# Optimization experiments

Hardware: AMD Instinct MI355X
Metric: run time of the kernel (lower is better)

## Reference

```python
import jax, jax.numpy as jnp
import numpy as np
from jax import lax

MB, NS, Z_DIM, R_DIM, HID, NUM_STEPS = 128, 64, 64, 128, 512, 100
B = MB * NS
T_TOTAL = 1.0
ETA = 1.0
DT = T_TOTAL / NUM_STEPS
LOG2PI = float(np.log(2.0 * np.pi))


def setup_inputs() -> dict:
    key = jax.random.key(0)
    ks = jax.random.split(key, 8)
    in_dim = Z_DIM + R_DIM + 1
    return {
        "r": jax.random.normal(ks[0], (MB, NS, R_DIM), jnp.float32),
        "noises": jax.random.normal(ks[1], (B, NUM_STEPS, Z_DIM), jnp.float32),
        "x0": jax.random.normal(ks[2], (B, Z_DIM), jnp.float32) * ETA,  # prior sample, std=eta
        "W1": jax.random.normal(ks[3], (in_dim, HID), jnp.float32) / np.sqrt(in_dim),
        "b1": jnp.zeros((HID,), jnp.float32),
        "W2": jax.random.normal(ks[4], (HID, Z_DIM), jnp.float32) / np.sqrt(HID),
        "b2": jnp.zeros((Z_DIM,), jnp.float32),
        "beta_max": jnp.float32(10.0),
        "beta_min": jnp.float32(0.01),
        "target_mu": jax.random.normal(ks[5], (Z_DIM,), jnp.float32),
    }


def reference(r, noises, x0, W1, b1, W2, b2, beta_max, beta_min, target_mu):
    # cosine-squared schedule (analytic integrals), per update_schedules()
    C_start = jax.nn.softplus(beta_max)
    C_end = jax.nn.softplus(beta_min)
    a = C_start - C_end
    b = jnp.pi / (2.0 * T_TOTAL)
    c = C_end

    def F(t):  # forward integrated scheduler \int_0^t
        return a * jnp.sin(2.0 * b * t) / (4.0 * b) + a * t / 2.0 + c * t

    steps = jnp.arange(NUM_STEPS + 1, dtype=jnp.float32)
    alpha = 1.0 - jnp.exp(-2.0 * (F((steps + 1.0) * DT) - F(steps * DT)))  # [S+1]
    kappa = (ETA * (1.0 - jnp.sqrt(1.0 - alpha))) ** 2 / alpha              # [S+1]

    r_flat = r.reshape(B, R_DIM)

    def control(t, x):  # score network: MLP on concat(x, r, t)
        t_feat = jnp.full((B, 1), t, dtype=x.dtype)
        h = jnp.tanh(jnp.concatenate([x, r_flat, t_feat], axis=-1) @ W1 + b1)
        return h @ W2 + b2

    def step(carry, xs):
        x, lw = carry
        t, al, ka, noise = xs
        score = control(t, x)
        means = x + (1.0 - jnp.sqrt(1.0 - al)) * (2.0 * ETA ** 2 * score - x)
        std = ETA * jnp.sqrt(al)
        x_new = means + std * noise
        lw_det = -2.0 * ka * jnp.sum(score ** 2, axis=-1)
        lw_sto = -2.0 * jnp.sqrt(ka) * jnp.sum(score * noise, axis=-1)
        return (x_new, lw + lw_det + lw_sto), x_new

    xs = (
        jnp.arange(NUM_STEPS, dtype=jnp.float32) * DT,
        alpha[:NUM_STEPS],
        kappa[:NUM_STEPS],
        jnp.swapaxes(noises, 0, 1),  # [S, B, D]
    )
    (x, lw), x_hist = lax.scan(step, (x0, jnp.zeros((B,), x0.dtype)), xs)

    x_t = jnp.swapaxes(jnp.concatenate([x0[None], x_hist], axis=0), 0, 1)  # [B, S+1, D]

    # terminal weight: log target - log prior (both diagonal Normals)
    target_lp = jnp.sum(-0.5 * (x - target_mu) ** 2 - 0.5 * LOG2PI, axis=-1)
    prior_lp = jnp.sum(-0.5 * (x / ETA) ** 2 - 0.5 * LOG2PI - jnp.log(jnp.float32(ETA)), axis=-1)
    log_weights = lw + target_lp - prior_lp

    # nabla_g = prior_score(x) - target_score(x)
    nabla_g = (-x / ETA ** 2) - (-(x - target_mu))
    return x_t, log_weights, nabla_g
```

## Files before the change

kernel.cpp:

```cpp
#include <hip/hip_runtime.h>

#define ZD 64
#define RD 128
#define HIDDEN 512
#define NSTEP 100
#define OUT_PITCH 6464
#define DT_F 0.01f
#define ROWS 32

static const size_t LW_OFF = 52953088ull;
static const size_t NG_OFF = 52961280ull;

typedef __attribute__((ext_vector_type(2))) float  f32x2;
typedef __attribute__((ext_vector_type(4))) float  f32x4;
typedef __attribute__((ext_vector_type(8))) __bf16 bf16x8;
typedef __attribute__((ext_vector_type(2))) short  s16x2;
typedef __attribute__((ext_vector_type(4))) short  s16x4;
typedef __attribute__((ext_vector_type(8))) short  s16x8;

__device__ __forceinline__ short f2bs(float f) {
    return __builtin_bit_cast(short, (__bf16)f);
}
__device__ __forceinline__ float tanh_fast(float x) {
    float e = __builtin_amdgcn_exp2f(x * 2.88539008177793f);
    float r = __builtin_amdgcn_rcpf(e + 1.0f);
    return fmaf(-2.0f, r, 1.0f);
}

__global__ __launch_bounds__(1024, 1)
void sim_kernel(
    const float* __restrict__ r, const float* __restrict__ noises,
    const float* __restrict__ x0, const float* __restrict__ W1,
    const float* __restrict__ b1, const float* __restrict__ W2,
    const float* __restrict__ b2, const float* __restrict__ bmax,
    const float* __restrict__ bmin, const float* __restrict__ mu,
    float* __restrict__ out)
{
    __shared__ float Ps[2][ROWS][68];
    __shared__ unsigned short Xb[ROWS * 64];
    __shared__ unsigned short Hs[ROWS * HIDDEN];
    __shared__ float w1ts[HIDDEN];
    __shared__ float mus[ZD];
    __shared__ float b2s[ZD];
    __shared__ float tT[NSTEP], tG[NSTEP], tSd[NSTEP], tCd[NSTEP], tCs[NSTEP];

    const int tid  = threadIdx.x;
    const int lane = tid & 63;
    const int wave = tid >> 6;
    const int g4   = lane >> 4;
    const int l16  = lane & 15;
    const int row0 = blockIdx.x * ROWS;

    if (tid < NSTEP) {
        float spmax = log1pf(expf(bmax[0]));
        float spmin = log1pf(expf(bmin[0]));
        float a_ = spmax - spmin;
        float c_ = spmin;
        const float PI_ = 3.14159265358979323846f;
        float k = (float)tid;
        float t0 = k * DT_F, t1 = (k + 1.0f) * DT_F;
        float inv2pi = 1.0f / (2.0f * PI_);
        float F0 = a_ * sinf(PI_ * t0) * inv2pi + (0.5f * a_ + c_) * t0;
        float F1 = a_ * sinf(PI_ * t1) * inv2pi + (0.5f * a_ + c_) * t1;
        float al = 1.0f - expf(-2.0f * (F1 - F0));
        float gg = 1.0f - sqrtf(1.0f - al);
        float kap = (gg * gg) / al;
        tT[tid] = t0; tG[tid] = gg; tSd[tid] = sqrtf(al);
        tCd[tid] = -2.0f * kap; tCs[tid] = -2.0f * sqrtf(kap);
    }
    if (tid < HIDDEN) w1ts[tid] = W1[(size_t)192 * HIDDEN + tid];
    if (tid < ZD) { mus[tid] = mu[tid]; b2s[tid] = b2[tid]; }

    const int urow = tid >> 5;
    const int c2   = (tid & 31) * 2;
    const size_t ubase = (size_t)(row0 + urow);
    float xr0, xr1;
    {
        f32x2 v = *(const f32x2*)(x0 + ubase * ZD + c2);
        xr0 = v[0]; xr1 = v[1];
        *(f32x2*)(out + ubase * OUT_PITCH + c2) = v;
        s16x2 xv; xv[0] = f2bs(xr0); xv[1] = f2bs(xr1);
        *(s16x2*)(Xb + ((urow * 64 + c2) ^ ((urow & 7) << 3))) = xv;
    }

    f32x4 pref[2][2];
    {
        #pragma unroll
        for (int mt = 0; mt < 2; ++mt) {
            bf16x8 rf[4];
            const float* rp = r + (size_t)(row0 + mt * 16 + l16) * RD;
            #pragma unroll
            for (int kc = 0; kc < 4; ++kc) {
                f32x4 lo = *(const f32x4*)(rp + kc * 32 + g4 * 8);
                f32x4 hi = *(const f32x4*)(rp + kc * 32 + g4 * 8 + 4);
                bf16x8 v;
                v[0]=(__bf16)lo[0]; v[1]=(__bf16)lo[1]; v[2]=(__bf16)lo[2]; v[3]=(__bf16)lo[3];
                v[4]=(__bf16)hi[0]; v[5]=(__bf16)hi[1]; v[6]=(__bf16)hi[2]; v[7]=(__bf16)hi[3];
                rf[kc] = v;
            }
            #pragma unroll
            for (int j2 = 0; j2 < 2; ++j2) {
                int n  = (wave * 2 + j2) * 16 + l16;
                int n0 = (wave * 2 + j2) * 16 + g4 * 4;
                f32x4 acc = *(const f32x4*)(b1 + n0);
                #pragma unroll
                for (int kc = 0; kc < 4; ++kc) {
                    bf16x8 w;
                    #pragma unroll
                    for (int j = 0; j < 8; ++j)
                        w[j] = (__bf16)W1[(size_t)(64 + kc * 32 + g4 * 8 + j) * HIDDEN + n];
                    acc = __builtin_amdgcn_mfma_f32_16x16x32_bf16(w, rf[kc], acc, 0, 0, 0);
                }
                pref[j2][mt] = acc;
            }
        }
    }

    bf16x8 w1f[2][2];
    #pragma unroll
    for (int j2 = 0; j2 < 2; ++j2) {
        int n = (wave * 2 + j2) * 16 + l16;
        #pragma unroll
        for (int kc = 0; kc < 2; ++kc) {
            bf16x8 v;
            #pragma unroll
            for (int j = 0; j < 8; ++j) {
                int kk = kc * 32 + g4 * 8 + j;
                v[j] = (__bf16)W1[(size_t)kk * HIDDEN + n];
            }
            w1f[j2][kc] = v;
        }
    }
    const int zt = wave & 3, kh = (wave >> 2) & 1, mt2 = wave >> 3;
    bf16x8 w2f[8];
    {
        int n = zt * 16 + l16;
        #pragma unroll
        for (int i = 0; i < 8; ++i) {
            int kc = kh * 8 + i;
            bf16x8 v;
            #pragma unroll
            for (int j = 0; j < 8; ++j) {
                int kk = kc * 32 + g4 * 8 + j;
                v[j] = (__bf16)W2[(size_t)kk * ZD + n];
            }
            w2f[i] = v;
        }
    }

    float lw_acc = 0.0f;

    __syncthreads();

    for (int s = 0; s < NSTEP; ++s) {
        float t = tT[s], gg = tG[s], sdv = tSd[s], cd = tCd[s], cs = tCs[s];
        f32x2 nz = *(const f32x2*)(noises + (ubase * NSTEP + s) * ZD + c2);

        {
            s16x8 xb[2][2];
            #pragma unroll
            for (int mt = 0; mt < 2; ++mt) {
                int m = mt * 16 + l16;
                int swz = (m & 7) << 3;
                xb[mt][0] = *(const s16x8*)(Xb + ((m * 64 + g4 * 8) ^ swz));
                xb[mt][1] = *(const s16x8*)(Xb + ((m * 64 + 32 + g4 * 8) ^ swz));
            }
            #pragma unroll
            for (int j2 = 0; j2 < 2; ++j2) {
                int n0 = (wave * 2 + j2) * 16 + g4 * 4;
                f32x4 wt = *(const f32x4*)(w1ts + n0);
                #pragma unroll
                for (int mt = 0; mt < 2; ++mt) {
                    f32x4 acc = pref[j2][mt];
                    acc[0] = fmaf(t, wt[0], acc[0]);
                    acc[1] = fmaf(t, wt[1], acc[1]);
                    acc[2] = fmaf(t, wt[2], acc[2]);
                    acc[3] = fmaf(t, wt[3], acc[3]);
                    acc = __builtin_amdgcn_mfma_f32_16x16x32_bf16(
                        w1f[j2][0], __builtin_bit_cast(bf16x8, xb[mt][0]), acc, 0, 0, 0);
                    acc = __builtin_amdgcn_mfma_f32_16x16x32_bf16(
                        w1f[j2][1], __builtin_bit_cast(bf16x8, xb[mt][1]), acc, 0, 0, 0);
                    s16x4 hv;
                    hv[0] = f2bs(tanh_fast(acc[0]));
                    hv[1] = f2bs(tanh_fast(acc[1]));
                    hv[2] = f2bs(tanh_fast(acc[2]));
                    hv[3] = f2bs(tanh_fast(acc[3]));
                    int m = mt * 16 + l16;
                    *(s16x4*)(Hs + ((m * HIDDEN + n0) ^ ((m & 7) << 3))) = hv;
                }
            }
        }
        __syncthreads();

        {
            int m = mt2 * 16 + l16;
            int swz = (m & 7) << 3;
            f32x4 accA = { 0.f, 0.f, 0.f, 0.f };
            f32x4 accB = { 0.f, 0.f, 0.f, 0.f };
            int base = m * HIDDEN + kh * 256 + g4 * 8;
            #pragma unroll
            for (int i = 0; i < 8; i += 2) {
                s16x8 h0 = *(const s16x8*)(Hs + ((base + i * 32) ^ swz));
                accA = __builtin_amdgcn_mfma_f32_16x16x32_bf16(
                    w2f[i], __builtin_bit_cast(bf16x8, h0), accA, 0, 0, 0);
                s16x8 h1 = *(const s16x8*)(Hs + ((base + (i + 1) * 32) ^ swz));
                accB = __builtin_amdgcn_mfma_f32_16x16x32_bf16(
                    w2f[i + 1], __builtin_bit_cast(bf16x8, h1), accB, 0, 0, 0);
            }
            accA[0] += accB[0]; accA[1] += accB[1];
            accA[2] += accB[2]; accA[3] += accB[3];
            *(f32x4*)(&Ps[kh][m][zt * 16 + g4 * 4]) = accA;
        }
        __syncthreads();

        {
            f32x2 p0 = *(const f32x2*)(&Ps[0][urow][c2]);
            f32x2 p1 = *(const f32x2*)(&Ps[1][urow][c2]);
            f32x2 bb = *(const f32x2*)(&b2s[c2]);
            float s0 = p0[0] + p1[0] + bb[0];
            float s1 = p0[1] + p1[1] + bb[1];
            float xn0 = xr0 + gg * (2.0f * s0 - xr0) + sdv * nz[0];
            float xn1 = xr1 + gg * (2.0f * s1 - xr1) + sdv * nz[1];
            xr0 = xn0; xr1 = xn1;
            f32x2 xv = { xn0, xn1 };
            *(f32x2*)(out + ubase * OUT_PITCH + (size_t)(s + 1) * ZD + c2) = xv;
            s16x2 xb2; xb2[0] = f2bs(xn0); xb2[1] = f2bs(xn1);
            *(s16x2*)(Xb + ((urow * 64 + c2) ^ ((urow & 7) << 3))) = xb2;
            float v = cd * (s0 * s0 + s1 * s1) + cs * (s0 * nz[0] + s1 * nz[1]);
            v += __shfl_xor(v, 1, 64);
            v += __shfl_xor(v, 2, 64);
            v += __shfl_xor(v, 4, 64);
            v += __shfl_xor(v, 8, 64);
            v += __shfl_xor(v, 16, 64);
            lw_acc += v;
        }
        __syncthreads();
    }

    {
        float m0 = mus[c2], m1 = mus[c2 + 1];
        float d0 = xr0 - m0, d1 = xr1 - m1;
        f32x2 ng = { d0 - xr0, d1 - xr1 };
        *(f32x2*)(out + NG_OFF + ubase * ZD + c2) = ng;
        float part = 0.5f * (xr0 * xr0 + xr1 * xr1) - 0.5f * (d0 * d0 + d1 * d1);
        part += __shfl_xor(part, 1, 64);
        part += __shfl_xor(part, 2, 64);
        part += __shfl_xor(part, 4, 64);
        part += __shfl_xor(part, 8, 64);
        part += __shfl_xor(part, 16, 64);
        if ((tid & 31) == 0) out[LW_OFF + ubase] = lw_acc + part;
    }
}

extern "C" void kernel_launch(void* const* d_in, const int* in_sizes, int n_in,
                              void* d_out, int out_size, void* d_ws, size_t ws_size,
                              hipStream_t stream) {
    const float* r      = (const float*)d_in[0];
    const float* noises = (const float*)d_in[1];
    const float* x0     = (const float*)d_in[2];
    const float* W1     = (const float*)d_in[3];
    const float* b1     = (const float*)d_in[4];
    const float* W2     = (const float*)d_in[5];
    const float* b2     = (const float*)d_in[6];
    const float* bmax   = (const float*)d_in[7];
    const float* bmin   = (const float*)d_in[8];
    const float* mu     = (const float*)d_in[9];
    float* out = (float*)d_out;

    sim_kernel<<<256, 1024, 0, stream>>>(r, noises, x0, W1, b1, W2, b2,
                                         bmax, bmin, mu, out);
}
```

Baseline: 260.8 us.

## Split second GEMM over four K-quarters and defer log-weight reduction

Reworks how the 16 waves split the H@W2 GEMM. Each wave now covers two output column tiles over a quarter of K, so one LDS read of H feeds two MFMAs, and partial results go to four partial buffers instead of two. The per-step cross-lane shuffle reduction of the log-weight term is dropped: each lane keeps a private sum and the reduction happens once at the end. b2 and mu are read straight into registers, which removes their LDS staging. The epilogue now reads four partial buffers per step instead of two, and summation order changes slightly.

```diff
diff --git a/kernel.cpp b/kernel.cpp
--- a/kernel.cpp
+++ b/kernel.cpp
@@ -36,12 +36,10 @@
     const float* __restrict__ bmin, const float* __restrict__ mu,
     float* __restrict__ out)
 {
-    __shared__ float Ps[2][ROWS][68];
+    __shared__ float Ps[4][ROWS][72];
     __shared__ unsigned short Xb[ROWS * 64];
     __shared__ unsigned short Hs[ROWS * HIDDEN];
     __shared__ float w1ts[HIDDEN];
-    __shared__ float mus[ZD];
-    __shared__ float b2s[ZD];
     __shared__ float tT[NSTEP], tG[NSTEP], tSd[NSTEP], tCd[NSTEP], tCs[NSTEP];
 
     const int tid  = threadIdx.x;
@@ -69,7 +67,6 @@
         tCd[tid] = -2.0f * kap; tCs[tid] = -2.0f * sqrtf(kap);
     }
     if (tid < HIDDEN) w1ts[tid] = W1[(size_t)192 * HIDDEN + tid];
-    if (tid < ZD) { mus[tid] = mu[tid]; b2s[tid] = b2[tid]; }
 
     const int urow = tid >> 5;
     const int c2   = (tid & 31) * 2;
@@ -82,13 +79,14 @@
         s16x2 xv; xv[0] = f2bs(xr0); xv[1] = f2bs(xr1);
         *(s16x2*)(Xb + ((urow * 64 + c2) ^ ((urow & 7) << 3))) = xv;
     }
+    const float bb0 = b2[c2], bb1 = b2[c2 + 1];
 
     f32x4 pref[2][2];
     {
         #pragma unroll
-        for (int mt = 0; mt < 2; ++mt) {
+        for (int mtt = 0; mtt < 2; ++mtt) {
             bf16x8 rf[4];
-            const float* rp = r + (size_t)(row0 + mt * 16 + l16) * RD;
+            const float* rp = r + (size_t)(row0 + mtt * 16 + l16) * RD;
             #pragma unroll
             for (int kc = 0; kc < 4; ++kc) {
                 f32x4 lo = *(const f32x4*)(rp + kc * 32 + g4 * 8);
@@ -111,7 +109,7 @@
                         w[j] = (__bf16)W1[(size_t)(64 + kc * 32 + g4 * 8 + j) * HIDDEN + n];
                     acc = __builtin_amdgcn_mfma_f32_16x16x32_bf16(w, rf[kc], acc, 0, 0, 0);
                 }
-                pref[j2][mt] = acc;
+                pref[j2][mtt] = acc;
             }
         }
     }
@@ -131,61 +129,59 @@
             w1f[j2][kc] = v;
         }
     }
-    const int zt = wave & 3, kh = (wave >> 2) & 1, mt2 = wave >> 3;
-    bf16x8 w2f[8];
-    {
-        int n = zt * 16 + l16;
+    const int zh = wave & 1, kq = (wave >> 1) & 3, mtw = wave >> 3;
+    bf16x8 w2f[2][4];
+    #pragma unroll
+    for (int zt2 = 0; zt2 < 2; ++zt2) {
+        int n = (zh * 2 + zt2) * 16 + l16;
         #pragma unroll
-        for (int i = 0; i < 8; ++i) {
-            int kc = kh * 8 + i;
+        for (int i = 0; i < 4; ++i) {
             bf16x8 v;
             #pragma unroll
-            for (int j = 0; j < 8; ++j) {
-                int kk = kc * 32 + g4 * 8 + j;
-                v[j] = (__bf16)W2[(size_t)kk * ZD + n];
-            }
-            w2f[i] = v;
-        }
-    }
-
-    float lw_acc = 0.0f;
+            for (int j = 0; j < 8; ++j)
+                v[j] = (__bf16)W2[(size_t)(kq * 128 + i * 32 + g4 * 8 + j) * ZD + n];
+            w2f[zt2][i] = v;
+        }
+    }
+
+    float lwacc = 0.0f;
 
     __syncthreads();
 
     for (int s = 0; s < NSTEP; ++s) {
-        float t = tT[s], gg = tG[s], sdv = tSd[s], cd = tCd[s], cs = tCs[s];
+        float t = tT[s];
         f32x2 nz = *(const f32x2*)(noises + (ubase * NSTEP + s) * ZD + c2);
 
         {
             s16x8 xb[2][2];
             #pragma unroll
-            for (int mt = 0; mt < 2; ++mt) {
-                int m = mt * 16 + l16;
+            for (int mtt = 0; mtt < 2; ++mtt) {
+                int m = mtt * 16 + l16;
                 int swz = (m & 7) << 3;
-                xb[mt][0] = *(const s16x8*)(Xb + ((m * 64 + g4 * 8) ^ swz));
-                xb[mt][1] = *(const s16x8*)(Xb + ((m * 64 + 32 + g4 * 8) ^ swz));
+                xb[mtt][0] = *(const s16x8*)(Xb + ((m * 64 + g4 * 8) ^ swz));
+                xb[mtt][1] = *(const s16x8*)(Xb + ((m * 64 + 32 + g4 * 8) ^ swz));
             }
             #pragma unroll
             for (int j2 = 0; j2 < 2; ++j2) {
                 int n0 = (wave * 2 + j2) * 16 + g4 * 4;
                 f32x4 wt = *(const f32x4*)(w1ts + n0);
                 #pragma unroll
-                for (int mt = 0; mt < 2; ++mt) {
-                    f32x4 acc = pref[j2][mt];
+                for (int mtt = 0; mtt < 2; ++mtt) {
+                    f32x4 acc = pref[j2][mtt];
                     acc[0] = fmaf(t, wt[0], acc[0]);
                     acc[1] = fmaf(t, wt[1], acc[1]);
                     acc[2] = fmaf(t, wt[2], acc[2]);
                     acc[3] = fmaf(t, wt[3], acc[3]);
                     acc = __builtin_amdgcn_mfma_f32_16x16x32_bf16(
-                        w1f[j2][0], __builtin_bit_cast(bf16x8, xb[mt][0]), acc, 0, 0, 0);
+                        w1f[j2][0], __builtin_bit_cast(bf16x8, xb[mtt][0]), acc, 0, 0, 0);
                     acc = __builtin_amdgcn_mfma_f32_16x16x32_bf16(
-                        w1f[j2][1], __builtin_bit_cast(bf16x8, xb[mt][1]), acc, 0, 0, 0);
+                        w1f[j2][1], __builtin_bit_cast(bf16x8, xb[mtt][1]), acc, 0, 0, 0);
                     s16x4 hv;
                     hv[0] = f2bs(tanh_fast(acc[0]));
                     hv[1] = f2bs(tanh_fast(acc[1]));
                     hv[2] = f2bs(tanh_fast(acc[2]));
                     hv[3] = f2bs(tanh_fast(acc[3]));
-                    int m = mt * 16 + l16;
+                    int m = mtt * 16 + l16;
                     *(s16x4*)(Hs + ((m * HIDDEN + n0) ^ ((m & 7) << 3))) = hv;
                 }
             }
@@ -193,32 +189,32 @@
         __syncthreads();
 
         {
-            int m = mt2 * 16 + l16;
+            int m = mtw * 16 + l16;
             int swz = (m & 7) << 3;
-            f32x4 accA = { 0.f, 0.f, 0.f, 0.f };
-            f32x4 accB = { 0.f, 0.f, 0.f, 0.f };
-            int base = m * HIDDEN + kh * 256 + g4 * 8;
-            #pragma unroll
-            for (int i = 0; i < 8; i += 2) {
-                s16x8 h0 = *(const s16x8*)(Hs + ((base + i * 32) ^ swz));
-                accA = __builtin_amdgcn_mfma_f32_16x16x32_bf16(
-                    w2f[i], __builtin_bit_cast(bf16x8, h0), accA, 0, 0, 0);
-                s16x8 h1 = *(const s16x8*)(Hs + ((base + (i + 1) * 32) ^ swz));
-                accB = __builtin_amdgcn_mfma_f32_16x16x32_bf16(
-                    w2f[i + 1], __builtin_bit_cast(bf16x8, h1), accB, 0, 0, 0);
-            }
-            accA[0] += accB[0]; accA[1] += accB[1];
-            accA[2] += accB[2]; accA[3] += accB[3];
-            *(f32x4*)(&Ps[kh][m][zt * 16 + g4 * 4]) = accA;
+            int base = m * HIDDEN + kq * 128 + g4 * 8;
+            f32x4 aA = { 0.f, 0.f, 0.f, 0.f };
+            f32x4 aB = { 0.f, 0.f, 0.f, 0.f };
+            #pragma unroll
+            for (int i = 0; i < 4; ++i) {
+                s16x8 h = *(const s16x8*)(Hs + ((base + i * 32) ^ swz));
+                aA = __builtin_amdgcn_mfma_f32_16x16x32_bf16(
+                    w2f[0][i], __builtin_bit_cast(bf16x8, h), aA, 0, 0, 0);
+                aB = __builtin_amdgcn_mfma_f32_16x16x32_bf16(
+                    w2f[1][i], __builtin_bit_cast(bf16x8, h), aB, 0, 0, 0);
+            }
+            *(f32x4*)(&Ps[kq][m][(zh * 2 + 0) * 16 + g4 * 4]) = aA;
+            *(f32x4*)(&Ps[kq][m][(zh * 2 + 1) * 16 + g4 * 4]) = aB;
         }
         __syncthreads();
 
         {
+            float gg = tG[s], sdv = tSd[s], cd = tCd[s], cs = tCs[s];
             f32x2 p0 = *(const f32x2*)(&Ps[0][urow][c2]);
             f32x2 p1 = *(const f32x2*)(&Ps[1][urow][c2]);
-            f32x2 bb = *(const f32x2*)(&b2s[c2]);
-            float s0 = p0[0] + p1[0] + bb[0];
-            float s1 = p0[1] + p1[1] + bb[1];
+            f32x2 p2 = *(const f32x2*)(&Ps[2][urow][c2]);
+            f32x2 p3 = *(const f32x2*)(&Ps[3][urow][c2]);
+            float s0 = ((p0[0] + p1[0]) + (p2[0] + p3[0])) + bb0;
+            float s1 = ((p0[1] + p1[1]) + (p2[1] + p3[1])) + bb1;
             float xn0 = xr0 + gg * (2.0f * s0 - xr0) + sdv * nz[0];
             float xn1 = xr1 + gg * (2.0f * s1 - xr1) + sdv * nz[1];
             xr0 = xn0; xr1 = xn1;
@@ -226,29 +222,24 @@
             *(f32x2*)(out + ubase * OUT_PITCH + (size_t)(s + 1) * ZD + c2) = xv;
             s16x2 xb2; xb2[0] = f2bs(xn0); xb2[1] = f2bs(xn1);
             *(s16x2*)(Xb + ((urow * 64 + c2) ^ ((urow & 7) << 3))) = xb2;
-            float v = cd * (s0 * s0 + s1 * s1) + cs * (s0 * nz[0] + s1 * nz[1]);
-            v += __shfl_xor(v, 1, 64);
-            v += __shfl_xor(v, 2, 64);
-            v += __shfl_xor(v, 4, 64);
-            v += __shfl_xor(v, 8, 64);
-            v += __shfl_xor(v, 16, 64);
-            lw_acc += v;
+            lwacc += cd * (s0 * s0 + s1 * s1) + cs * (s0 * nz[0] + s1 * nz[1]);
         }
         __syncthreads();
     }
 
     {
-        float m0 = mus[c2], m1 = mus[c2 + 1];
+        float m0 = mu[c2], m1 = mu[c2 + 1];
         float d0 = xr0 - m0, d1 = xr1 - m1;
         f32x2 ng = { d0 - xr0, d1 - xr1 };
         *(f32x2*)(out + NG_OFF + ubase * ZD + c2) = ng;
-        float part = 0.5f * (xr0 * xr0 + xr1 * xr1) - 0.5f * (d0 * d0 + d1 * d1);
+        float part = lwacc
+                   + 0.5f * (xr0 * xr0 + xr1 * xr1) - 0.5f * (d0 * d0 + d1 * d1);
         part += __shfl_xor(part, 1, 64);
         part += __shfl_xor(part, 2, 64);
         part += __shfl_xor(part, 4, 64);
         part += __shfl_xor(part, 8, 64);
         part += __shfl_xor(part, 16, 64);
-        if ((tid & 31) == 0) out[LW_OFF + ubase] = lw_acc + part;
+        if ((tid & 31) == 0) out[LW_OFF + ubase] = part;
     }
 }
 
```

Result: faster. 241.2 us (-7.5%).
